# Performance work log

Hardware: AMD Instinct MI355X
Metric: run time of the kernel (lower is better)

The kernel has to match this reference:

```python
import jax, jax.numpy as jnp
import numpy as np

# Static per-expert capacities (tokens are laid out contiguously per expert)
CAPS = [1024, 512, 1024, 256, 1024, 512, 128, 1024, 512, 1024, 256, 512, 1024, 128, 64, 512]
TOTAL = sum(CAPS)  # 9536
E, H, I = 16, 1024, 4096
OFFSETS = np.concatenate([[0], np.cumsum(CAPS)])


def setup_inputs() -> dict:
    key = jax.random.key(0)
    ks = jax.random.split(key, 5)
    x = jax.random.normal(ks[0], (TOTAL, H), dtype=jnp.float32)
    W1 = jax.random.normal(ks[1], (E, I, H), dtype=jnp.float32) * 0.02
    b1 = jax.random.normal(ks[2], (E, I), dtype=jnp.float32) * 0.02
    W2 = jax.random.normal(ks[3], (E, H, I), dtype=jnp.float32) * 0.02
    b2 = jax.random.normal(ks[4], (E, H), dtype=jnp.float32) * 0.02
    return {"x": x, "W1": W1, "b1": b1, "W2": W2, "b2": b2}


def reference(x, W1, b1, W2, b2):
    # Grouped GEMM FFN: expert e processes rows [OFFSETS[e]:OFFSETS[e+1]]
    # out = gelu(x_e @ W1[e].T + b1[e]) @ W2[e].T + b2[e]
    outs = []
    for e in range(E):  # fixed, static loop over experts (capacities are static)
        xs = x[OFFSETS[e]:OFFSETS[e + 1]]                      # [cap_e, H]
        h = jax.nn.gelu(xs @ W1[e].T + b1[e], approximate=False)  # [cap_e, I]
        outs.append(h @ W2[e].T + b2[e])                       # [cap_e, H]
    return jnp.concatenate(outs, axis=0)                       # [TOTAL, H]
```

## Files before the change

### kernel.cpp

```cpp
#include <hip/hip_runtime.h>
#include <math.h>

typedef __attribute__((ext_vector_type(8))) short short8;
typedef __attribute__((ext_vector_type(4))) float f32x4;
typedef __attribute__((ext_vector_type(2))) unsigned int u32x2;

#define E_NUM 16
constexpr int CAPS[E_NUM] = {1024,512,1024,256,1024,512,128,1024,512,1024,256,512,1024,128,64,512};
constexpr int OFFS[E_NUM] = {0,1024,1536,2560,2816,3840,4352,4480,5504,6016,7040,7296,7808,8832,8960,9024};
constexpr int cdiv_(int a, int b){ return (a + b - 1) / b; }
constexpr int ilog2_(int v){ int l = 0; while ((1 << l) < v) ++l; return l; }

__device__ __forceinline__ unsigned int cvt_pk_bf16(float a, float b){
  unsigned int r;
  asm("v_cvt_pk_bf16_f32 %0, %1, %2" : "=v"(r) : "v"(a), "v"(b));
  return r;
}

typedef __attribute__((address_space(1))) const unsigned char gas_u8;
typedef __attribute__((address_space(3))) unsigned char las_u8;
__device__ __forceinline__ void gl_lds16(const void* g, void* l){
  __builtin_amdgcn_global_load_lds((gas_u8*)g, (las_u8*)l, 16, 0, 0);
}

__global__ __launch_bounds__(256) void cvt_bf16_kernel(const float* __restrict__ x,
                                                       unsigned short* __restrict__ xb, int n8)
{
  int i = blockIdx.x * blockDim.x + threadIdx.x;
  const int stride = gridDim.x * blockDim.x;
  for (; i < n8; i += stride) {
    f32x4 a = *reinterpret_cast<const f32x4*>(x + (size_t)i * 8);
    f32x4 b = *reinterpret_cast<const f32x4*>(x + (size_t)i * 8 + 4);
    u32x2 lo, hi;
    lo[0] = cvt_pk_bf16(a[0], a[1]); lo[1] = cvt_pk_bf16(a[2], a[3]);
    hi[0] = cvt_pk_bf16(b[0], b[1]); hi[1] = cvt_pk_bf16(b[2], b[3]);
    *reinterpret_cast<u32x2*>(xb + (size_t)i * 8)     = lo;
    *reinterpret_cast<u32x2*>(xb + (size_t)i * 8 + 4) = hi;
  }
}

template<bool A_GLDS, bool GELU_OUT, int TM, int NDIM, int KDIM, int LOG_GN, int NWG>
__global__ __launch_bounds__(256, 4)
void expert_gemm(const void* __restrict__ Av, const float* __restrict__ W,
                 const float* __restrict__ bias, void* __restrict__ Outv)
{
  constexpr int A_SZ = TM * 32;
  constexpr int B_SZ = 128 * 32;
  constexpr int GN   = 1 << LOG_GN;
  constexpr int MFR  = TM / 32;
  static_assert(NWG % 8 == 0, "grid must be divisible by 8 for XCD swizzle");
  static_assert(!GELU_OUT || 2 * (A_SZ + B_SZ) >= 128 * 128, "GELU transpose needs 32KB");

  __shared__ __align__(16) unsigned short smem[2 * A_SZ + 2 * B_SZ];

  const int tid  = threadIdx.x;
  const int braw = blockIdx.x;
  const int t = (braw & 7) * (NWG / 8) + (braw >> 3);

  int m0 = 0, n0 = 0, Me = 0, tok0 = 0;
  size_t wbase = 0, bbase = 0;
  {
    int acc0 = 0;
    #pragma unroll
    for (int i = 0; i < E_NUM; ++i) {
      const int mt  = cdiv_(CAPS[i], TM);
      const int lmt = ilog2_(mt);
      const int nb  = mt * (NDIM / 128);
      if (t >= acc0 && t < acc0 + nb) {
        const int loc = t - acc0;
        const int g   = loc >> (lmt + LOG_GN);
        const int rem = loc & ((mt << LOG_GN) - 1);
        m0   = (rem >> LOG_GN) * TM;
        n0   = ((g << LOG_GN) | (rem & (GN - 1))) * 128;
        Me   = CAPS[i];
        tok0 = OFFS[i];
        wbase = (size_t)i * NDIM * KDIM;
        bbase = (size_t)i * NDIM;
      }
      acc0 += nb;
    }
  }
  const float* Wb = W + wbase;

  const int lane = tid & 63;
  const int wv   = tid >> 6;
  const int sr   = tid >> 3;
  const int sc   = (tid & 7) * 8;
  const int spc  = sc ^ ((sr & 3) << 4);

  const unsigned short* Ah = (const unsigned short*)Av;
  const float*          Af = (const float*)Av;

  f32x4 ra[MFR]; f32x4 rb[4];

  auto loadB = [&](int kt) {
    const int k0 = kt * 32;
    #pragma unroll
    for (int i = 0; i < 4; ++i)
      rb[i] = *reinterpret_cast<const f32x4*>(Wb + (size_t)(n0 + sr + 32 * i) * KDIM + k0 + (sc >> 1));
  };
  auto writeB = [&](int buf) {
    char* bb = (char*)(smem + 2 * A_SZ + buf * B_SZ);
    #pragma unroll
    for (int i = 0; i < 4; ++i) {
      u32x2 p;
      p[0] = cvt_pk_bf16(rb[i][0], rb[i][1]);
      p[1] = cvt_pk_bf16(rb[i][2], rb[i][3]);
      *reinterpret_cast<u32x2*>(bb + (sr + 32 * i) * 64 + spc) = p;
    }
  };

  auto stageA_glds = [&](int buf, int kt) {
    constexpr int AI = TM / 64;
    const unsigned short* Ag = Ah + (size_t)(tok0 + m0) * KDIM + kt * 32;
    #pragma unroll
    for (int j = 0; j < AI; ++j) {
      const int rbase = wv * (AI * 16) + j * 16;
      const int r     = rbase + (lane >> 2);
      const int gblk  = (lane & 3) ^ (r & 3);
      gl_lds16((const void*)(Ag + (size_t)r * KDIM + gblk * 8),
               (void*)(smem + buf * A_SZ + rbase * 32));
    }
  };
  auto loadA_reg = [&](int kt) {
    const int k0 = kt * 32;
    #pragma unroll
    for (int i = 0; i < MFR; ++i)
      ra[i] = *reinterpret_cast<const f32x4*>(Af + (size_t)(tok0 + m0 + sr + 32 * i) * KDIM + k0 + (sc >> 1));
  };
  auto writeA_reg = [&](int buf) {
    char* ab = (char*)(smem + buf * A_SZ);
    #pragma unroll
    for (int i = 0; i < MFR; ++i) {
      u32x2 p;
      p[0] = cvt_pk_bf16(ra[i][0], ra[i][1]);
      p[1] = cvt_pk_bf16(ra[i][2], ra[i][3]);
      *reinterpret_cast<u32x2*>(ab + (sr + 32 * i) * 64 + spc) = p;
    }
  };

  const int wm   = (wv >> 1) * (TM / 2);
  const int wn   = (wv & 1) * 64;
  const int lrow = lane & 15;
  const int fcs  = ((lane >> 4) << 4) ^ ((lane & 3) << 4);

  f32x4 acc_[MFR][4];
  #pragma unroll
  for (int i = 0; i < MFR; ++i)
    #pragma unroll
    for (int j = 0; j < 4; ++j)
      acc_[i][j] = (f32x4){0.f, 0.f, 0.f, 0.f};

  loadB(0);
  if constexpr (A_GLDS) stageA_glds(0, 0); else { loadA_reg(0); writeA_reg(0); }
  writeB(0);
  __syncthreads();

  constexpr int NT = KDIM / 32;
  for (int kt = 0; kt < NT; ++kt) {
    const int cur = kt & 1;
    if (kt + 1 < NT) {
      loadB(kt + 1);
      if constexpr (A_GLDS) stageA_glds(cur ^ 1, kt + 1);
      else                  loadA_reg(kt + 1);
    }

    const char* ab = (const char*)(smem + cur * A_SZ);
    const char* bb = (const char*)(smem + 2 * A_SZ + cur * B_SZ);
    short8 afr[MFR], bfr[4];
    #pragma unroll
    for (int f = 0; f < MFR; ++f)
      afr[f] = *reinterpret_cast<const short8*>(ab + (wm + f * 16 + lrow) * 64 + fcs);
    #pragma unroll
    for (int f = 0; f < 4; ++f)
      bfr[f] = *reinterpret_cast<const short8*>(bb + (wn + f * 16 + lrow) * 64 + fcs);

    #pragma unroll
    for (int i = 0; i < MFR; ++i)
      #pragma unroll
      for (int j = 0; j < 4; ++j)
        acc_[i][j] = __builtin_amdgcn_mfma_f32_16x16x32_bf16(afr[i], bfr[j], acc_[i][j], 0, 0, 0);

    if (kt + 1 < NT) {
      writeB(cur ^ 1);
      if constexpr (!A_GLDS) writeA_reg(cur ^ 1);
    }
    __syncthreads();
  }

  float bv[4];
  #pragma unroll
  for (int f = 0; f < 4; ++f)
    bv[f] = bias[bbase + n0 + wn + f * 16 + lrow];

  if constexpr (GELU_OUT) {
    static_assert(TM == 128, "GELU path assumes 128-row tiles");
    unsigned short* hout = smem;
    #pragma unroll
    for (int i = 0; i < MFR; ++i) {
      const int rbase = wm + i * 16 + (lane >> 4) * 4;
      #pragma unroll
      for (int j = 0; j < 4; ++j) {
        #pragma unroll
        for (int jj = 0; jj < 4; ++jj) {
          float xv = acc_[i][j][jj] + bv[j];
          float g  = 0.5f * xv * (1.0f + erff(xv * 0.70710678118654752f));
          hout[(rbase + jj) * 128 + wn + j * 16 + lrow] = (unsigned short)(cvt_pk_bf16(g, g) & 0xFFFFu);
        }
      }
    }
    __syncthreads();
    unsigned short* Oh = (unsigned short*)Outv;
    #pragma unroll
    for (int it = 0; it < 8; ++it) {
      int row  = it * 16 + (tid >> 4);
      int c    = (tid & 15) * 8;
      int grow = m0 + row;
      if (grow < Me) {
        *reinterpret_cast<short8*>(Oh + (size_t)(tok0 + grow) * NDIM + n0 + c)
          = *reinterpret_cast<const short8*>(hout + row * 128 + c);
      }
    }
  } else {
    float* Of = (float*)Outv;
    #pragma unroll
    for (int i = 0; i < MFR; ++i) {
      const int rbase = wm + i * 16 + (lane >> 4) * 4;
      #pragma unroll
      for (int jj = 0; jj < 4; ++jj) {
        int grow = m0 + rbase + jj;
        if (grow < Me) {
          #pragma unroll
          for (int j = 0; j < 4; ++j) {
            Of[(size_t)(tok0 + grow) * NDIM + n0 + wn + j * 16 + lrow] = acc_[i][j][jj] + bv[j];
          }
        }
      }
    }
  }
}

extern "C" void kernel_launch(void* const* d_in, const int* in_sizes, int n_in,
                              void* d_out, int out_size, void* d_ws, size_t ws_size,
                              hipStream_t stream)
{
  const float* x  = (const float*)d_in[0];
  const float* W1 = (const float*)d_in[1];
  const float* b1 = (const float*)d_in[2];
  const float* W2 = (const float*)d_in[3];
  const float* b2 = (const float*)d_in[4];
  float* out = (float*)d_out;

  constexpr size_t H_BYTES  = (size_t)9536 * 4096 * 2;
  constexpr size_t XB_BYTES = (size_t)9536 * 1024 * 2;
  unsigned short* h  = (unsigned short*)d_ws;
  unsigned short* xb = (unsigned short*)((char*)d_ws + H_BYTES);

  const bool use_xb = ws_size >= H_BYTES + XB_BYTES;

  if (use_xb) {
    cvt_bf16_kernel<<<2048, 256, 0, stream>>>(x, xb, 9536 * 1024 / 8);
    expert_gemm<true, true, 128, 4096, 1024, 2, 75 * 32>
        <<<75 * 32, 256, 0, stream>>>((const void*)xb, W1, b1, (void*)h);
  } else {
    expert_gemm<false, true, 128, 4096, 1024, 2, 75 * 32>
        <<<75 * 32, 256, 0, stream>>>((const void*)x, W1, b1, (void*)h);
  }

  expert_gemm<true, false, 64, 1024, 4096, 0, 149 * 8>
      <<<149 * 8, 256, 0, stream>>>((const void*)h, W2, b2, (void*)out);
}
```

Before: 398.2 us.

## Deepen B-prefetch pipeline with explicit waitcnt barriers, raise occupancy, approximate GELU

In the global-load-to-LDS path, the K loop is unrolled by two with two register sets for W tiles, so the B load runs two K-steps ahead. Custom barriers wait only on older vector loads (vmcnt(4)) instead of draining all memory operations, which should hide more global latency. Launch bounds are raised to 8 waves per SIMD, which may force register spilling. Exact erf-based GELU is replaced by a tanh-style sigmoid approximation, which is cheaper but deviates from the reference's exact GELU.

```diff
diff --git a/kernel.cpp b/kernel.cpp
--- a/kernel.cpp
+++ b/kernel.cpp
@@ -21,6 +21,17 @@
 typedef __attribute__((address_space(3))) unsigned char las_u8;
 __device__ __forceinline__ void gl_lds16(const void* g, void* l){
   __builtin_amdgcn_global_load_lds((gas_u8*)g, (las_u8*)l, 16, 0, 0);
+}
+
+__device__ __forceinline__ void bar_vm4(){
+  __builtin_amdgcn_sched_barrier(0);
+  asm volatile("s_waitcnt vmcnt(4) lgkmcnt(0)\n\ts_barrier" ::: "memory");
+  __builtin_amdgcn_sched_barrier(0);
+}
+__device__ __forceinline__ void bar_vm0(){
+  __builtin_amdgcn_sched_barrier(0);
+  asm volatile("s_waitcnt vmcnt(0) lgkmcnt(0)\n\ts_barrier" ::: "memory");
+  __builtin_amdgcn_sched_barrier(0);
 }
 
 __global__ __launch_bounds__(256) void cvt_bf16_kernel(const float* __restrict__ x,
@@ -40,7 +51,7 @@
 }
 
 template<bool A_GLDS, bool GELU_OUT, int TM, int NDIM, int KDIM, int LOG_GN, int NWG>
-__global__ __launch_bounds__(256, 4)
+__global__ __launch_bounds__(256, 8)
 void expert_gemm(const void* __restrict__ Av, const float* __restrict__ W,
                  const float* __restrict__ bias, void* __restrict__ Outv)
 {
@@ -48,6 +59,8 @@
   constexpr int B_SZ = 128 * 32;
   constexpr int GN   = 1 << LOG_GN;
   constexpr int MFR  = TM / 32;
+  constexpr int NT   = KDIM / 32;
+  static_assert(NT % 2 == 0, "unroll-2 pipeline needs even NT");
   static_assert(NWG % 8 == 0, "grid must be divisible by 8 for XCD swizzle");
   static_assert(!GELU_OUT || 2 * (A_SZ + B_SZ) >= 128 * 128, "GELU transpose needs 32KB");
 
@@ -91,15 +104,13 @@
   const unsigned short* Ah = (const unsigned short*)Av;
   const float*          Af = (const float*)Av;
 
-  f32x4 ra[MFR]; f32x4 rb[4];
-
-  auto loadB = [&](int kt) {
+  auto loadB = [&](int kt, f32x4 (&rb)[4]) {
     const int k0 = kt * 32;
     #pragma unroll
     for (int i = 0; i < 4; ++i)
       rb[i] = *reinterpret_cast<const f32x4*>(Wb + (size_t)(n0 + sr + 32 * i) * KDIM + k0 + (sc >> 1));
   };
-  auto writeB = [&](int buf) {
+  auto writeB = [&](int buf, f32x4 (&rb)[4]) {
     char* bb = (char*)(smem + 2 * A_SZ + buf * B_SZ);
     #pragma unroll
     for (int i = 0; i < 4; ++i) {
@@ -122,13 +133,13 @@
                (void*)(smem + buf * A_SZ + rbase * 32));
     }
   };
-  auto loadA_reg = [&](int kt) {
+  auto loadA_reg = [&](int kt, f32x4 (&ra)[MFR]) {
     const int k0 = kt * 32;
     #pragma unroll
     for (int i = 0; i < MFR; ++i)
       ra[i] = *reinterpret_cast<const f32x4*>(Af + (size_t)(tok0 + m0 + sr + 32 * i) * KDIM + k0 + (sc >> 1));
   };
-  auto writeA_reg = [&](int buf) {
+  auto writeA_reg = [&](int buf, f32x4 (&ra)[MFR]) {
     char* ab = (char*)(smem + buf * A_SZ);
     #pragma unroll
     for (int i = 0; i < MFR; ++i) {
@@ -151,20 +162,7 @@
     for (int j = 0; j < 4; ++j)
       acc_[i][j] = (f32x4){0.f, 0.f, 0.f, 0.f};
 
-  loadB(0);
-  if constexpr (A_GLDS) stageA_glds(0, 0); else { loadA_reg(0); writeA_reg(0); }
-  writeB(0);
-  __syncthreads();
-
-  constexpr int NT = KDIM / 32;
-  for (int kt = 0; kt < NT; ++kt) {
-    const int cur = kt & 1;
-    if (kt + 1 < NT) {
-      loadB(kt + 1);
-      if constexpr (A_GLDS) stageA_glds(cur ^ 1, kt + 1);
-      else                  loadA_reg(kt + 1);
-    }
-
+  auto mfma_step = [&](int cur) {
     const char* ab = (const char*)(smem + cur * A_SZ);
     const char* bb = (const char*)(smem + 2 * A_SZ + cur * B_SZ);
     short8 afr[MFR], bfr[4];
@@ -174,18 +172,46 @@
     #pragma unroll
     for (int f = 0; f < 4; ++f)
       bfr[f] = *reinterpret_cast<const short8*>(bb + (wn + f * 16 + lrow) * 64 + fcs);
-
     #pragma unroll
     for (int i = 0; i < MFR; ++i)
       #pragma unroll
       for (int j = 0; j < 4; ++j)
         acc_[i][j] = __builtin_amdgcn_mfma_f32_16x16x32_bf16(afr[i], bfr[j], acc_[i][j], 0, 0, 0);
-
-    if (kt + 1 < NT) {
-      writeB(cur ^ 1);
-      if constexpr (!A_GLDS) writeA_reg(cur ^ 1);
-    }
+  };
+
+  if constexpr (A_GLDS) {
+    f32x4 rb0[4], rb1[4];
+    loadB(0, rb0);
+    stageA_glds(0, 0);
+    writeB(0, rb0);
+    loadB(1, rb1);
+    bar_vm4();
+
+    auto body = [&](int kt, int cur, f32x4 (&rbW)[4], f32x4 (&rbL)[4]) {
+      if (kt + 1 < NT) {
+        stageA_glds(cur ^ 1, kt + 1);
+        writeB(cur ^ 1, rbW);
+      }
+      if (kt + 2 < NT) loadB(kt + 2, rbL);
+      mfma_step(cur);
+      if (kt + 2 < NT) bar_vm4(); else bar_vm0();
+    };
+    for (int kt = 0; kt < NT; kt += 2) {
+      body(kt,     0, rb1, rb0);
+      body(kt + 1, 1, rb0, rb1);
+    }
+  } else {
+    f32x4 rb0[4]; f32x4 ra[MFR];
+    loadB(0, rb0); loadA_reg(0, ra);
+    writeB(0, rb0); writeA_reg(0, ra);
     __syncthreads();
+    for (int kt = 0; kt < NT; ++kt) {
+      const int cur = kt & 1;
+      if (kt + 1 < NT) { loadB(kt + 1, rb0); loadA_reg(kt + 1, ra); }
+      mfma_step(cur);
+      if (kt + 1 < NT) { writeB(cur ^ 1, rb0); writeA_reg(cur ^ 1, ra); }
+      __syncthreads();
+    }
   }
 
   float bv[4];
@@ -204,7 +230,8 @@
         #pragma unroll
         for (int jj = 0; jj < 4; ++jj) {
           float xv = acc_[i][j][jj] + bv[j];
-          float g  = 0.5f * xv * (1.0f + erff(xv * 0.70710678118654752f));
+          float y2 = xv * (1.5957691216057308f + 0.07135481627f * xv * xv);
+          float g  = xv * __builtin_amdgcn_rcpf(1.0f + __expf(-y2));
           hout[(rbase + jj) * 128 + wn + j * 16 + lrow] = (unsigned short)(cvt_pk_bf16(g, g) & 0xFFFFu);
         }
       }
```

Measured after the change: 427.8 us. +7.4%, slower.
